# Kernel optimization log

Measured on AMD Instinct MI355X. Metric: run time of the kernel, lower is better.

Reference implementation:

```python
import jax, jax.numpy as jnp
import numpy as np

B, T, C, H = 4, 2048, 1024, 16


def setup_inputs() -> dict:
    key = jax.random.key(0)
    k0, k1, k2 = jax.random.split(key, 3)
    s = C ** -0.5
    return {
        "x": jax.random.normal(k0, (B, T, C), jnp.float32),
        "Wqkv": jax.random.normal(k1, (C, 3 * C), jnp.float32) * s,
        "bqkv": jnp.zeros((3 * C,), jnp.float32),
        "Wo": jax.random.normal(k2, (C, C), jnp.float32) * s,
        "bo": jnp.zeros((C,), jnp.float32),
        "decoder": 1,
    }


def reference(x, Wqkv, bqkv, Wo, bo, decoder):
    Bx, Tx, Cx = x.shape
    d = Cx // H  # head dim
    qkv = x @ Wqkv + bqkv  # [B,T,3C]
    q, k, v = jnp.split(qkv, 3, axis=-1)
    q = q.reshape(Bx, Tx, H, d).transpose(0, 2, 1, 3)  # [B,H,T,d]
    k = k.reshape(Bx, Tx, H, d).transpose(0, 2, 1, 3)
    v = v.reshape(Bx, Tx, H, d).transpose(0, 2, 1, 3)
    # Source: qk / embd_dim**(-0.5)  ==  qk * sqrt(embd_dim)  (faithful quirk)
    scale = jnp.asarray(Cx ** 0.5, x.dtype)
    qk = jnp.einsum("bhqd,bhkd->bhqk", q, k) * scale  # [B,H,T,T]
    if decoder:  # decoder is a Python int constant
        tril = jnp.tril(jnp.ones((Tx, Tx), bool))
        qk = jnp.where(tril, qk, -jnp.inf)
    attn = jax.nn.softmax(qk, axis=-1)
    out = jnp.einsum("bhqk,bhkd->bhqd", attn, v)  # [B,H,T,d]
    out = out.transpose(0, 2, 1, 3).reshape(Bx, Tx, Cx)
    return out @ Wo + bo
```

## Files before the change

kernel.cpp:

```cpp
#include <hip/hip_runtime.h>
#include <cstdint>
#include <cstddef>

#define T_SEQ 2048
#define CEMB  1024
#define NHEAD 16
#define DHEAD 64

#define QSCALE 46.1662413084468f

typedef __attribute__((ext_vector_type(8))) short bf16x8;
typedef __attribute__((ext_vector_type(4))) float f32x4;

static __device__ __forceinline__ unsigned short f2bf(float x) {
    unsigned u = __builtin_bit_cast(unsigned, x);
    unsigned r = (u + 0x7FFFu + ((u >> 16) & 1u)) >> 16;
    return (unsigned short)r;
}
static __device__ __forceinline__ float bf2f(unsigned short b) {
    unsigned u = ((unsigned)b) << 16;
    return __builtin_bit_cast(float, u);
}

static __device__ __forceinline__ void gload16(const short* gsrc, short* ldsbase) {
    __builtin_amdgcn_global_load_lds(
        (const __attribute__((address_space(1))) void*)gsrc,
        (__attribute__((address_space(3))) void*)ldsbase, 16, 0, 0);
}

__global__ __launch_bounds__(256) void split_x_kernel(
    const float* __restrict__ x, short* __restrict__ hi, short* __restrict__ lo)
{
    size_t base = ((size_t)blockIdx.x * 256 + threadIdx.x) * 8;
    float4 f0 = *(const float4*)(x + base);
    float4 f1 = *(const float4*)(x + base + 4);
    float xs[8] = {f0.x, f0.y, f0.z, f0.w, f1.x, f1.y, f1.z, f1.w};
    bf16x8 h8, l8;
    #pragma unroll
    for (int e = 0; e < 8; ++e) {
        unsigned u = __builtin_bit_cast(unsigned, xs[e]);
        h8[e] = (short)(unsigned short)(u >> 16);
        float hf = __builtin_bit_cast(float, u & 0xFFFF0000u);
        l8[e] = (short)f2bf(xs[e] - hf);
    }
    *(bf16x8*)(hi + base) = h8;
    *(bf16x8*)(lo + base) = l8;
}

__global__ __launch_bounds__(512) void gemm_qk_kernel(
    const short* __restrict__ Ah, const short* __restrict__ Al,
    const short* __restrict__ Bh, const short* __restrict__ Bl,
    const float* __restrict__ bias,
    short* __restrict__ Chi, short* __restrict__ Clo, int K)
{
    __shared__ __align__(16) short smem[24576];

    const int tid = threadIdx.x;
    const int wv = tid >> 6, l = tid & 63;
    const int lr = l & 15, lg = l >> 4;
    const int wr = wv >> 1, wc = wv & 1;
    const int row0 = blockIdx.y * 256;
    const int col0 = blockIdx.x * 128;

    f32x4 acc[4][4];
    #pragma unroll
    for (int mt = 0; mt < 4; ++mt)
        #pragma unroll
        for (int nt = 0; nt < 4; ++nt)
            acc[mt][nt] = (f32x4){0.f, 0.f, 0.f, 0.f};

    const int sA0 = wv * 128 + l, sA1 = sA0 + 64;
    const size_t aO0 = (size_t)(row0 + (sA0 & 255)) * K + (sA0 >> 8) * 8;
    const size_t aO1 = (size_t)(row0 + (sA1 & 255)) * K + (sA1 >> 8) * 8;
    const int sB = wv * 64 + l;
    const size_t bO = (size_t)(col0 + (sB & 127)) * K + (sB >> 7) * 8;

    const short* gAh0 = Ah + aO0;  const short* gAh1 = Ah + aO1;
    const short* gAl0 = Al + aO0;  const short* gAl1 = Al + aO1;
    const short* gBh  = Bh + bO;   const short* gBl  = Bl + bO;

    short* const dA0 = &smem[(wv * 128) * 8];
    short* const dA1 = &smem[(wv * 128 + 64) * 8];
    short* const dB  = &smem[16384 + (wv * 64) * 8];

    for (int kt = 0; kt < K; kt += 32) {
        __syncthreads();
        gload16(gAh0 + kt, dA0);
        gload16(gAh1 + kt, dA1);
        gload16(gAl0 + kt, dA0 + 8192);
        gload16(gAl1 + kt, dA1 + 8192);
        gload16(gBh + kt, dB);
        gload16(gBl + kt, dB + 4096);
        __syncthreads();

        const int ao = (lg * 256 + wr * 64 + lr) * 8;
        const int bo = 16384 + (lg * 128 + wc * 64 + lr) * 8;
        bf16x8 ahf[4], alf[4];
        #pragma unroll
        for (int mt = 0; mt < 4; ++mt) {
            ahf[mt] = *(const bf16x8*)&smem[ao + mt * 128];
            alf[mt] = *(const bf16x8*)&smem[8192 + ao + mt * 128];
        }
        #pragma unroll
        for (int nt = 0; nt < 4; ++nt) {
            bf16x8 bhf = *(const bf16x8*)&smem[bo + nt * 128];
            bf16x8 blf = *(const bf16x8*)&smem[4096 + bo + nt * 128];
            #pragma unroll
            for (int mt = 0; mt < 4; ++mt) {
                acc[mt][nt] = __builtin_amdgcn_mfma_f32_16x16x32_bf16(ahf[mt], bhf, acc[mt][nt], 0, 0, 0);
                acc[mt][nt] = __builtin_amdgcn_mfma_f32_16x16x32_bf16(alf[mt], bhf, acc[mt][nt], 0, 0, 0);
                acc[mt][nt] = __builtin_amdgcn_mfma_f32_16x16x32_bf16(ahf[mt], blf, acc[mt][nt], 0, 0, 0);
            }
        }
    }

    #pragma unroll
    for (int mt = 0; mt < 4; ++mt) {
        #pragma unroll
        for (int r = 0; r < 4; ++r) {
            int m = row0 + wr * 64 + mt * 16 + lg * 4 + r;
            #pragma unroll
            for (int nt = 0; nt < 4; ++nt) {
                int n = col0 + wc * 64 + nt * 16 + lr;
                float v = acc[mt][nt][r] + bias[n];
                if (n < 1024) v *= QSCALE;
                unsigned u = __builtin_bit_cast(unsigned, v);
                Chi[(size_t)m * 2048 + n] = (short)(unsigned short)(u >> 16);
                float hf = __builtin_bit_cast(float, u & 0xFFFF0000u);
                Clo[(size_t)m * 2048 + n] = (short)f2bf(v - hf);
            }
        }
    }
}

__global__ __launch_bounds__(256) void gemm_v_kernel(
    const short* __restrict__ Ah, const short* __restrict__ Bh,
    const float* __restrict__ bias, short* __restrict__ vt, int K)
{
    __shared__ __align__(16) short smem[17408];

    const int tid = threadIdx.x;
    const int w = tid >> 6, l = tid & 63;
    const int lr = l & 15, lg = l >> 4;
    const int wr = w >> 1, wc = w & 1;
    const int row0 = blockIdx.y * 128;
    const int col0 = blockIdx.x * 128;

    f32x4 acc[4][4];
    #pragma unroll
    for (int mt = 0; mt < 4; ++mt)
        #pragma unroll
        for (int nt = 0; nt < 4; ++nt)
            acc[mt][nt] = (f32x4){0.f, 0.f, 0.f, 0.f};

    const int s0 = w * 128 + l, s1 = s0 + 64;
    const size_t aoff0 = (size_t)(row0 + (s0 & 127)) * K + (s0 >> 7) * 8;
    const size_t aoff1 = (size_t)(row0 + (s1 & 127)) * K + (s1 >> 7) * 8;
    const size_t boff0 = (size_t)(col0 + (s0 & 127)) * K + (s0 >> 7) * 8;
    const size_t boff1 = (size_t)(col0 + (s1 & 127)) * K + (s1 >> 7) * 8;
    const short* gA0 = Ah + aoff0;  const short* gA1 = Ah + aoff1;
    const short* gB0 = Bh + boff0;  const short* gB1 = Bh + boff1;
    short* const dA0 = &smem[(w * 128) * 8];
    short* const dA1 = &smem[(w * 128 + 64) * 8];
    short* const dB0 = &smem[4096 + (w * 128) * 8];
    short* const dB1 = &smem[4096 + (w * 128 + 64) * 8];

    for (int kt = 0; kt < K; kt += 32) {
        __syncthreads();
        gload16(gA0 + kt, dA0);
        gload16(gA1 + kt, dA1);
        gload16(gB0 + kt, dB0);
        gload16(gB1 + kt, dB1);
        __syncthreads();

        const int ao = (lg * 128 + wr * 64 + lr) * 8;
        const int bo = 4096 + (lg * 128 + wc * 64 + lr) * 8;
        bf16x8 ahf[4];
        #pragma unroll
        for (int mt = 0; mt < 4; ++mt)
            ahf[mt] = *(const bf16x8*)&smem[ao + mt * 128];
        #pragma unroll
        for (int nt = 0; nt < 4; ++nt) {
            bf16x8 bhf = *(const bf16x8*)&smem[bo + nt * 128];
            #pragma unroll
            for (int mt = 0; mt < 4; ++mt)
                acc[mt][nt] = __builtin_amdgcn_mfma_f32_16x16x32_bf16(ahf[mt], bhf, acc[mt][nt], 0, 0, 0);
        }
    }

    __syncthreads();
    #pragma unroll
    for (int mt = 0; mt < 4; ++mt) {
        const int tb = wr * 64 + mt * 16 + lg * 4;
        #pragma unroll
        for (int nt = 0; nt < 4; ++nt) {
            const int nl = wc * 64 + nt * 16 + lr;
            float v0 = acc[mt][nt][0] + bias[col0 + nl];
            float v1 = acc[mt][nt][1] + bias[col0 + nl];
            float v2 = acc[mt][nt][2] + bias[col0 + nl];
            float v3 = acc[mt][nt][3] + bias[col0 + nl];
            unsigned u0 = (unsigned)f2bf(v0) | ((unsigned)f2bf(v1) << 16);
            unsigned u1 = (unsigned)f2bf(v2) | ((unsigned)f2bf(v3) << 16);
            uint2 uu; uu.x = u0; uu.y = u1;
            *(uint2*)&smem[nl * 136 + tb] = uu;
        }
    }
    __syncthreads();

    const int b  = row0 >> 11;
    const int t0 = row0 & 2047;
    #pragma unroll
    for (int i = 0; i < 8; ++i) {
        int nl = (tid >> 4) + i * 16;
        int t8 = (tid & 15) * 8;
        bf16x8 vv = *(const bf16x8*)&smem[nl * 136 + t8];
        int n = col0 + nl;
        int hh = n >> 6, d = n & 63;
        short* dst = vt + ((size_t)((b * NHEAD + hh) * DHEAD + d)) * T_SEQ + t0 + t8;
        *(bf16x8*)dst = vv;
    }
}

__global__ __launch_bounds__(256) void gemm_proj_kernel(
    const short* __restrict__ Ah, const short* __restrict__ Bh,
    const float* __restrict__ bias, float* __restrict__ Cout, int K, int ldc)
{
    __shared__ __align__(16) short smem[8192];

    const int tid = threadIdx.x;
    const int w = tid >> 6, l = tid & 63;
    const int lr = l & 15, lg = l >> 4;
    const int wr = w >> 1, wc = w & 1;
    const int row0 = blockIdx.y * 128;
    const int col0 = blockIdx.x * 128;

    f32x4 acc[4][4];
    #pragma unroll
    for (int mt = 0; mt < 4; ++mt)
        #pragma unroll
        for (int nt = 0; nt < 4; ++nt)
            acc[mt][nt] = (f32x4){0.f, 0.f, 0.f, 0.f};

    const int s0 = w * 128 + l, s1 = s0 + 64;
    const size_t aoff0 = (size_t)(row0 + (s0 & 127)) * K + (s0 >> 7) * 8;
    const size_t aoff1 = (size_t)(row0 + (s1 & 127)) * K + (s1 >> 7) * 8;
    const size_t boff0 = (size_t)(col0 + (s0 & 127)) * K + (s0 >> 7) * 8;
    const size_t boff1 = (size_t)(col0 + (s1 & 127)) * K + (s1 >> 7) * 8;
    const short* gA0 = Ah + aoff0;  const short* gA1 = Ah + aoff1;
    const short* gB0 = Bh + boff0;  const short* gB1 = Bh + boff1;
    short* const dA0 = &smem[(w * 128) * 8];
    short* const dA1 = &smem[(w * 128 + 64) * 8];
    short* const dB0 = &smem[4096 + (w * 128) * 8];
    short* const dB1 = &smem[4096 + (w * 128 + 64) * 8];

    for (int kt = 0; kt < K; kt += 32) {
        __syncthreads();
        gload16(gA0 + kt, dA0);
        gload16(gA1 + kt, dA1);
        gload16(gB0 + kt, dB0);
        gload16(gB1 + kt, dB1);
        __syncthreads();

        const int ao = (lg * 128 + wr * 64 + lr) * 8;
        const int bo = 4096 + (lg * 128 + wc * 64 + lr) * 8;
        bf16x8 ahf[4];
        #pragma unroll
        for (int mt = 0; mt < 4; ++mt)
            ahf[mt] = *(const bf16x8*)&smem[ao + mt * 128];
        #pragma unroll
        for (int nt = 0; nt < 4; ++nt) {
            bf16x8 bhf = *(const bf16x8*)&smem[bo + nt * 128];
            #pragma unroll
            for (int mt = 0; mt < 4; ++mt)
                acc[mt][nt] = __builtin_amdgcn_mfma_f32_16x16x32_bf16(ahf[mt], bhf, acc[mt][nt], 0, 0, 0);
        }
    }

    #pragma unroll
    for (int mt = 0; mt < 4; ++mt) {
        #pragma unroll
        for (int r = 0; r < 4; ++r) {
            int m = row0 + wr * 64 + mt * 16 + lg * 4 + r;
            #pragma unroll
            for (int nt = 0; nt < 4; ++nt) {
                int n = col0 + wc * 64 + nt * 16 + lr;
                Cout[(size_t)m * ldc + n] = acc[mt][nt][r] + bias[n];
            }
        }
    }
}

__global__ __launch_bounds__(256) void transpose_split_kernel(
    const float* __restrict__ src, int nsrc,
    short* __restrict__ hi, short* __restrict__ lo)
{
    __shared__ float tile[64][68];
    const int tid = threadIdx.x;
    const int n0 = blockIdx.x * 64, k0 = blockIdx.y * 64;
    {
        int kr = tid >> 2, cg = tid & 3;
        const float* s = src + (size_t)(k0 + kr) * nsrc + n0 + cg * 16;
        #pragma unroll
        for (int q = 0; q < 4; ++q) {
            float4 f = *(const float4*)(s + q * 4);
            tile[kr][cg * 16 + q * 4 + 0] = f.x;
            tile[kr][cg * 16 + q * 4 + 1] = f.y;
            tile[kr][cg * 16 + q * 4 + 2] = f.z;
            tile[kr][cg * 16 + q * 4 + 3] = f.w;
        }
    }
    __syncthreads();
    {
        int nr = tid >> 2, kg = tid & 3;
        int n = n0 + nr;
        bf16x8 h0, h1, lo0, lo1;
        #pragma unroll
        for (int e = 0; e < 8; ++e) {
            float a = tile[kg * 16 + e][nr];
            float b = tile[kg * 16 + 8 + e][nr];
            unsigned short ha = f2bf(a), hb = f2bf(b);
            h0[e] = (short)ha; h1[e] = (short)hb;
            lo0[e] = (short)f2bf(a - bf2f(ha));
            lo1[e] = (short)f2bf(b - bf2f(hb));
        }
        short* dh = hi + (size_t)n * 1024 + k0 + kg * 16;
        *(bf16x8*)dh = h0;
        *(bf16x8*)(dh + 8) = h1;
        if (lo) {
            short* dl = lo + (size_t)n * 1024 + k0 + kg * 16;
            *(bf16x8*)dl = lo0;
            *(bf16x8*)(dl + 8) = lo1;
        }
    }
}

__global__ __launch_bounds__(256) void attn_mfma_kernel(
    const short* __restrict__ qkhi, const short* __restrict__ qklo,
    const short* __restrict__ vt, short* __restrict__ ctxb)
{
    __shared__ __align__(16) short smem[20480];

    const int tid = threadIdx.x;
    const int w = tid >> 6, l = tid & 63;
    const int lr = l & 15, lg = l >> 4;

    const int bid = blockIdx.x;
    const int p  = bid >> 6;
    const int bh = bid & 63;
    const int h = bh & 15, b = bh >> 4;
    const size_t bT = (size_t)b * T_SEQ;

    const int g0 = w * 128 + l, g1 = g0 + 64;
    const int rg0 = g0 >> 3, rg1 = g1 >> 3;
    const int sc0 = (g0 & 7) ^ (rg0 & 7), sc1 = (g1 & 7) ^ (rg1 & 7);
    short* const dK0 = &smem[(w * 128) * 8];
    short* const dK1 = &smem[(w * 128 + 64) * 8];

    const size_t koff0 = (bT + rg0) * 2048 + 1024 + h * DHEAD + sc0 * 8;
    const size_t koff1 = (bT + rg1) * 2048 + 1024 + h * DHEAD + sc1 * 8;
    const short* const pKh0 = qkhi + koff0;
    const short* const pKh1 = qkhi + koff1;
    const short* const pKl0 = qklo + koff0;
    const short* const pKl1 = qklo + koff1;
    const short* const pV0 = vt + ((size_t)((b * NHEAD + h) * DHEAD) + rg0) * T_SEQ + sc0 * 8;
    const short* const pV1 = vt + ((size_t)((b * NHEAD + h) * DHEAD) + rg1) * T_SEQ + sc1 * 8;

    const int psBase = 16384 + w * 1024;
    const int pwChunk = (lg >> 1);
    const int pwIntra = (lg & 1) * 4;

    for (int half = 0; half < 2; ++half) {
        const int xi = half ? (31 - p) : p;
        const int qw = xi * 64 + w * 16;
        const int nsteps = xi + 1;

        __syncthreads();

        bf16x8 qhi[2], qlo[2];
        #pragma unroll
        for (int kk = 0; kk < 2; ++kk) {
            size_t off = (bT + qw + lr) * 2048 + h * DHEAD + kk * 32 + lg * 8;
            qhi[kk] = *(const bf16x8*)(qkhi + off);
            qlo[kk] = *(const bf16x8*)(qklo + off);
        }
        __builtin_amdgcn_sched_barrier(0);

        gload16(pKh0, dK0);
        gload16(pKh1, dK1);
        gload16(pKl0, dK0 + 4096);
        gload16(pKl1, dK1 + 4096);
        gload16(pV0, dK0 + 8192);
        gload16(pV1, dK1 + 8192);
        {
            int j1 = (nsteps > 1) ? 64 : 0;
            gload16(pV0 + j1, dK0 + 12288);
            gload16(pV1 + j1, dK1 + 12288);
        }

        f32x4 O[4];
        #pragma unroll
        for (int dt = 0; dt < 4; ++dt)
            O[dt] = (f32x4){0.f, 0.f, 0.f, 0.f};
        float mrow = -3.0e38f;
        float lrow = 0.f;

        for (int t = 0; t < nsteps; ++t) {
            const int j0 = t * 64;
            asm volatile("s_waitcnt vmcnt(2)" ::: "memory");
            __builtin_amdgcn_s_barrier();
            __builtin_amdgcn_sched_barrier(0);
            const int vbase = 8192 + (t & 1) * 4096;

            f32x4 St[4];
            __builtin_amdgcn_s_setprio(1);
            #pragma unroll
            for (int ct = 0; ct < 4; ++ct) {
                f32x4 s = (f32x4){0.f, 0.f, 0.f, 0.f};
                #pragma unroll
                for (int kk = 0; kk < 2; ++kk) {
                    int j  = ct * 16 + lr;
                    int ck = kk * 4 + lg;
                    int idx = j * 64 + ((ck ^ (j & 7)) << 3);
                    bf16x8 kh8 = *(bf16x8*)&smem[idx];
                    bf16x8 kl8 = *(bf16x8*)&smem[4096 + idx];
                    s = __builtin_amdgcn_mfma_f32_16x16x32_bf16(kh8, qhi[kk], s, 0, 0, 0);
                    s = __builtin_amdgcn_mfma_f32_16x16x32_bf16(kh8, qlo[kk], s, 0, 0, 0);
                    s = __builtin_amdgcn_mfma_f32_16x16x32_bf16(kl8, qhi[kk], s, 0, 0, 0);
                }
                St[ct] = s;
            }
            __builtin_amdgcn_s_setprio(0);
            #pragma unroll
            for (int ct = 0; ct < 4; ++ct) {
                if (j0 + ct * 16 + 15 > qw) {
                    #pragma unroll
                    for (int r = 0; r < 4; ++r) {
                        int jabs = j0 + ct * 16 + lg * 4 + r;
                        St[ct][r] = (jabs <= qw + lr) ? St[ct][r] : -3.0e38f;
                    }
                }
            }

            float tm = fmaxf(fmaxf(fmaxf(St[0][0], St[0][1]), fmaxf(St[0][2], St[0][3])),
                             fmaxf(fmaxf(St[1][0], St[1][1]), fmaxf(St[1][2], St[1][3])));
            tm = fmaxf(tm, fmaxf(fmaxf(fmaxf(St[2][0], St[2][1]), fmaxf(St[2][2], St[2][3])),
                                 fmaxf(fmaxf(St[3][0], St[3][1]), fmaxf(St[3][2], St[3][3]))));
            tm = fmaxf(tm, __shfl_xor(tm, 16));
            tm = fmaxf(tm, __shfl_xor(tm, 32));

            if (__any(tm > mrow)) {
                float mnew  = fmaxf(mrow, tm);
                float alpha = __builtin_amdgcn_exp2f(mrow - mnew);
                mrow = mnew;
                lrow *= alpha;
                #pragma unroll
                for (int r = 0; r < 4; ++r) {
                    float aO = __shfl(alpha, lg * 4 + r);
                    #pragma unroll
                    for (int dt = 0; dt < 4; ++dt)
                        O[dt][r] *= aO;
                }
            }

            #pragma unroll
            for (int ct = 0; ct < 4; ++ct) {
                float p0 = __builtin_amdgcn_exp2f(St[ct][0] - mrow);
                float p1 = __builtin_amdgcn_exp2f(St[ct][1] - mrow);
                float p2 = __builtin_amdgcn_exp2f(St[ct][2] - mrow);
                float p3 = __builtin_amdgcn_exp2f(St[ct][3] - mrow);
                lrow += (p0 + p1) + (p2 + p3);
                unsigned u0 = (__builtin_bit_cast(unsigned, p0) >> 16) |
                              (__builtin_bit_cast(unsigned, p1) & 0xFFFF0000u);
                unsigned u1 = (__builtin_bit_cast(unsigned, p2) >> 16) |
                              (__builtin_bit_cast(unsigned, p3) & 0xFFFF0000u);
                int chunk = ct * 2 + pwChunk;
                int sidx = psBase + lr * 64 + ((chunk ^ (lr & 7)) << 3) + pwIntra;
                uint2 uu; uu.x = u0; uu.y = u1;
                *(uint2*)&smem[sidx] = uu;
            }

            __builtin_amdgcn_wave_barrier();

            bf16x8 pa[2];
            #pragma unroll
            for (int jk = 0; jk < 2; ++jk) {
                int ck = jk * 4 + lg;
                pa[jk] = *(bf16x8*)&smem[psBase + lr * 64 + ((ck ^ (lr & 7)) << 3)];
            }
            __builtin_amdgcn_s_setprio(1);
            #pragma unroll
            for (int dt = 0; dt < 4; ++dt) {
                #pragma unroll
                for (int jk = 0; jk < 2; ++jk) {
                    int d  = dt * 16 + lr;
                    int ck = jk * 4 + lg;
                    bf16x8 vb = *(bf16x8*)&smem[vbase + d * 64 + ((ck ^ (d & 7)) << 3)];
                    O[dt] = __builtin_amdgcn_mfma_f32_16x16x32_bf16(pa[jk], vb, O[dt], 0, 0, 0);
                }
            }
            __builtin_amdgcn_s_setprio(0);

            __builtin_amdgcn_sched_barrier(0);
            __builtin_amdgcn_s_barrier();
            __builtin_amdgcn_sched_barrier(0);

            if (t + 1 < nsteps) {
                size_t ko = (size_t)(t + 1) * 131072;
                gload16(pKh0 + ko, dK0);
                gload16(pKh1 + ko, dK1);
                gload16(pKl0 + ko, dK0 + 4096);
                gload16(pKl1 + ko, dK1 + 4096);
                int jv = (t + 2 < nsteps) ? (t + 2) : (nsteps - 1);
                short* const dV = &smem[8192 + (t & 1) * 4096];
                gload16(pV0 + jv * 64, dV + (w * 128) * 8);
                gload16(pV1 + jv * 64, dV + (w * 128 + 64) * 8);
            }
        }

        float lsum = lrow + __shfl_xor(lrow, 16);
        lsum += __shfl_xor(lsum, 32);
        #pragma unroll
        for (int r = 0; r < 4; ++r) {
            float lO = __shfl(lsum, lg * 4 + r);
            float inv = 1.0f / lO;
            int row = qw + lg * 4 + r;
            #pragma unroll
            for (int dt = 0; dt < 4; ++dt) {
                int col = h * DHEAD + dt * 16 + lr;
                ctxb[(size_t)(b * T_SEQ + row) * CEMB + col] = (short)f2bf(O[dt][r] * inv);
            }
        }
    }
}

extern "C" void kernel_launch(void* const* d_in, const int* in_sizes, int n_in,
                              void* d_out, int out_size, void* d_ws, size_t ws_size,
                              hipStream_t stream)
{
    const float* x    = (const float*)d_in[0];
    const float* Wqkv = (const float*)d_in[1];
    const float* bqkv = (const float*)d_in[2];
    const float* Wo   = (const float*)d_in[3];
    const float* bo   = (const float*)d_in[4];
    float* out = (float*)d_out;

    char* ws = (char*)d_ws;
    short* qkhi = (short*)ws;
    short* qklo = (short*)(ws + (size_t)(32u << 20));
    short* xlo  = (short*)(ws + (size_t)(64u << 20));
    short* Vt   = xlo;
    short* xhi  = (short*)(ws + (size_t)(80u << 20));
    short* ctxb = xhi;
    short* WhiT = (short*)(ws + (size_t)(96u << 20));
    short* WloT = (short*)(ws + (size_t)(102u << 20));
    short* WoT  = (short*)(ws + (size_t)(108u << 20));

    transpose_split_kernel<<<dim3(48, 16), 256, 0, stream>>>(Wqkv, 3 * CEMB, WhiT, WloT);
    transpose_split_kernel<<<dim3(16, 16), 256, 0, stream>>>(Wo, CEMB, WoT, nullptr);

    split_x_kernel<<<dim3(4096), 256, 0, stream>>>(x, xhi, xlo);

    gemm_qk_kernel<<<dim3(16, 32), 512, 0, stream>>>(
        xhi, xlo, WhiT, WloT, bqkv, qkhi, qklo, CEMB);

    gemm_v_kernel<<<dim3(8, 64), 256, 0, stream>>>(
        xhi, WhiT + (size_t)2048 * 1024, bqkv + 2048, Vt, CEMB);

    attn_mfma_kernel<<<dim3(1024), 256, 0, stream>>>(qkhi, qklo, Vt, ctxb);

    gemm_proj_kernel<<<dim3(8, 64), 256, 0, stream>>>(
        ctxb, WoT, bo, out, CEMB, CEMB);
}
```

Baseline: 395.3 us.

## Fuse fp32-to-bf16 x split into QK and V GEMM loads; double-buffer projection GEMM

Removes the separate split_x kernel. The QK and V GEMMs now read fp32 x directly and convert it to bf16 hi/lo (or rounded bf16 for V) in registers before writing to LDS. This saves a full write and re-read of the split x buffers. The QK GEMM tile shrinks from 256x128 with 512 threads to 128x128 with 256 threads. The projection GEMM gains a two-stage LDS double buffer with explicit waitcnt and barriers so loads overlap MFMA work. The A-side loads are now synchronous register loads with conversion work in the k-loop, which may add latency because they are no longer async global-to-LDS.

```diff
diff --git a/kernel.cpp b/kernel.cpp
--- a/kernel.cpp
+++ b/kernel.cpp
@@ -28,38 +28,19 @@
         (__attribute__((address_space(3))) void*)ldsbase, 16, 0, 0);
 }
 
-__global__ __launch_bounds__(256) void split_x_kernel(
-    const float* __restrict__ x, short* __restrict__ hi, short* __restrict__ lo)
-{
-    size_t base = ((size_t)blockIdx.x * 256 + threadIdx.x) * 8;
-    float4 f0 = *(const float4*)(x + base);
-    float4 f1 = *(const float4*)(x + base + 4);
-    float xs[8] = {f0.x, f0.y, f0.z, f0.w, f1.x, f1.y, f1.z, f1.w};
-    bf16x8 h8, l8;
-    #pragma unroll
-    for (int e = 0; e < 8; ++e) {
-        unsigned u = __builtin_bit_cast(unsigned, xs[e]);
-        h8[e] = (short)(unsigned short)(u >> 16);
-        float hf = __builtin_bit_cast(float, u & 0xFFFF0000u);
-        l8[e] = (short)f2bf(xs[e] - hf);
-    }
-    *(bf16x8*)(hi + base) = h8;
-    *(bf16x8*)(lo + base) = l8;
-}
-
-__global__ __launch_bounds__(512) void gemm_qk_kernel(
-    const short* __restrict__ Ah, const short* __restrict__ Al,
+__global__ __launch_bounds__(256) void gemm_qk_kernel(
+    const float* __restrict__ Af,
     const short* __restrict__ Bh, const short* __restrict__ Bl,
     const float* __restrict__ bias,
     short* __restrict__ Chi, short* __restrict__ Clo, int K)
 {
-    __shared__ __align__(16) short smem[24576];
+    __shared__ __align__(16) short smem[16384];
 
     const int tid = threadIdx.x;
-    const int wv = tid >> 6, l = tid & 63;
+    const int w = tid >> 6, l = tid & 63;
     const int lr = l & 15, lg = l >> 4;
-    const int wr = wv >> 1, wc = wv & 1;
-    const int row0 = blockIdx.y * 256;
+    const int wr = w >> 1, wc = w & 1;
+    const int row0 = blockIdx.y * 128;
     const int col0 = blockIdx.x * 128;
 
     f32x4 acc[4][4];
@@ -69,32 +50,51 @@
         for (int nt = 0; nt < 4; ++nt)
             acc[mt][nt] = (f32x4){0.f, 0.f, 0.f, 0.f};
 
-    const int sA0 = wv * 128 + l, sA1 = sA0 + 64;
-    const size_t aO0 = (size_t)(row0 + (sA0 & 255)) * K + (sA0 >> 8) * 8;
-    const size_t aO1 = (size_t)(row0 + (sA1 & 255)) * K + (sA1 >> 8) * 8;
-    const int sB = wv * 64 + l;
-    const size_t bO = (size_t)(col0 + (sB & 127)) * K + (sB >> 7) * 8;
-
-    const short* gAh0 = Ah + aO0;  const short* gAh1 = Ah + aO1;
-    const short* gAl0 = Al + aO0;  const short* gAl1 = Al + aO1;
-    const short* gBh  = Bh + bO;   const short* gBl  = Bl + bO;
-
-    short* const dA0 = &smem[(wv * 128) * 8];
-    short* const dA1 = &smem[(wv * 128 + 64) * 8];
-    short* const dB  = &smem[16384 + (wv * 64) * 8];
+    const int sB0 = w * 128 + l, sB1 = sB0 + 64;
+    const size_t bO0 = (size_t)(col0 + (sB0 & 127)) * K + (sB0 >> 7) * 8;
+    const size_t bO1 = (size_t)(col0 + (sB1 & 127)) * K + (sB1 >> 7) * 8;
+    const short* gB0  = Bh + bO0;  const short* gB1  = Bh + bO1;
+    const short* gBl0 = Bl + bO0;  const short* gBl1 = Bl + bO1;
+    short* const dB0 = &smem[4096 + (w * 128) * 8];
+    short* const dB1 = &smem[4096 + (w * 128 + 64) * 8];
+
+    const int arow = tid >> 1, ahalf = tid & 1;
+    const float* gAf = Af + (size_t)(row0 + arow) * K + ahalf * 16;
 
     for (int kt = 0; kt < K; kt += 32) {
         __syncthreads();
-        gload16(gAh0 + kt, dA0);
-        gload16(gAh1 + kt, dA1);
-        gload16(gAl0 + kt, dA0 + 8192);
-        gload16(gAl1 + kt, dA1 + 8192);
-        gload16(gBh + kt, dB);
-        gload16(gBl + kt, dB + 4096);
+        gload16(gB0 + kt, dB0);
+        gload16(gB1 + kt, dB1);
+        gload16(gBl0 + kt, dB0 + 8192);
+        gload16(gBl1 + kt, dB1 + 8192);
+        {
+            const float* src = gAf + kt;
+            float4 f0 = *(const float4*)(src);
+            float4 f1 = *(const float4*)(src + 4);
+            float4 f2 = *(const float4*)(src + 8);
+            float4 f3 = *(const float4*)(src + 12);
+            float xs[16] = {f0.x, f0.y, f0.z, f0.w, f1.x, f1.y, f1.z, f1.w,
+                            f2.x, f2.y, f2.z, f2.w, f3.x, f3.y, f3.z, f3.w};
+            #pragma unroll
+            for (int q = 0; q < 2; ++q) {
+                bf16x8 h8, l8;
+                #pragma unroll
+                for (int e = 0; e < 8; ++e) {
+                    float x = xs[q * 8 + e];
+                    unsigned u = __builtin_bit_cast(unsigned, x);
+                    h8[e] = (short)(unsigned short)(u >> 16);
+                    float hf = __builtin_bit_cast(float, u & 0xFFFF0000u);
+                    l8[e] = (short)f2bf(x - hf);
+                }
+                int slot = (ahalf * 2 + q) * 128 + arow;
+                *(bf16x8*)&smem[slot * 8] = h8;
+                *(bf16x8*)&smem[8192 + slot * 8] = l8;
+            }
+        }
         __syncthreads();
 
-        const int ao = (lg * 256 + wr * 64 + lr) * 8;
-        const int bo = 16384 + (lg * 128 + wc * 64 + lr) * 8;
+        const int ao = (lg * 128 + wr * 64 + lr) * 8;
+        const int bo = 4096 + (lg * 128 + wc * 64 + lr) * 8;
         bf16x8 ahf[4], alf[4];
         #pragma unroll
         for (int mt = 0; mt < 4; ++mt) {
@@ -104,7 +104,7 @@
         #pragma unroll
         for (int nt = 0; nt < 4; ++nt) {
             bf16x8 bhf = *(const bf16x8*)&smem[bo + nt * 128];
-            bf16x8 blf = *(const bf16x8*)&smem[4096 + bo + nt * 128];
+            bf16x8 blf = *(const bf16x8*)&smem[8192 + bo + nt * 128];
             #pragma unroll
             for (int mt = 0; mt < 4; ++mt) {
                 acc[mt][nt] = __builtin_amdgcn_mfma_f32_16x16x32_bf16(ahf[mt], bhf, acc[mt][nt], 0, 0, 0);
@@ -134,10 +134,110 @@
 }
 
 __global__ __launch_bounds__(256) void gemm_v_kernel(
-    const short* __restrict__ Ah, const short* __restrict__ Bh,
+    const float* __restrict__ Af, const short* __restrict__ Bh,
     const float* __restrict__ bias, short* __restrict__ vt, int K)
 {
     __shared__ __align__(16) short smem[17408];
+
+    const int tid = threadIdx.x;
+    const int w = tid >> 6, l = tid & 63;
+    const int lr = l & 15, lg = l >> 4;
+    const int wr = w >> 1, wc = w & 1;
+    const int row0 = blockIdx.y * 128;
+    const int col0 = blockIdx.x * 128;
+
+    f32x4 acc[4][4];
+    #pragma unroll
+    for (int mt = 0; mt < 4; ++mt)
+        #pragma unroll
+        for (int nt = 0; nt < 4; ++nt)
+            acc[mt][nt] = (f32x4){0.f, 0.f, 0.f, 0.f};
+
+    const int sB0 = w * 128 + l, sB1 = sB0 + 64;
+    const size_t bO0 = (size_t)(col0 + (sB0 & 127)) * K + (sB0 >> 7) * 8;
+    const size_t bO1 = (size_t)(col0 + (sB1 & 127)) * K + (sB1 >> 7) * 8;
+    const short* gB0 = Bh + bO0;  const short* gB1 = Bh + bO1;
+    short* const dB0 = &smem[4096 + (w * 128) * 8];
+    short* const dB1 = &smem[4096 + (w * 128 + 64) * 8];
+
+    const int arow = tid >> 1, ahalf = tid & 1;
+    const float* gAf = Af + (size_t)(row0 + arow) * K + ahalf * 16;
+
+    for (int kt = 0; kt < K; kt += 32) {
+        __syncthreads();
+        gload16(gB0 + kt, dB0);
+        gload16(gB1 + kt, dB1);
+        {
+            const float* src = gAf + kt;
+            float4 f0 = *(const float4*)(src);
+            float4 f1 = *(const float4*)(src + 4);
+            float4 f2 = *(const float4*)(src + 8);
+            float4 f3 = *(const float4*)(src + 12);
+            float xs[16] = {f0.x, f0.y, f0.z, f0.w, f1.x, f1.y, f1.z, f1.w,
+                            f2.x, f2.y, f2.z, f2.w, f3.x, f3.y, f3.z, f3.w};
+            #pragma unroll
+            for (int q = 0; q < 2; ++q) {
+                bf16x8 h8;
+                #pragma unroll
+                for (int e = 0; e < 8; ++e) h8[e] = (short)f2bf(xs[q * 8 + e]);
+                int slot = (ahalf * 2 + q) * 128 + arow;
+                *(bf16x8*)&smem[slot * 8] = h8;
+            }
+        }
+        __syncthreads();
+
+        const int ao = (lg * 128 + wr * 64 + lr) * 8;
+        const int bo = 4096 + (lg * 128 + wc * 64 + lr) * 8;
+        bf16x8 ahf[4];
+        #pragma unroll
+        for (int mt = 0; mt < 4; ++mt)
+            ahf[mt] = *(const bf16x8*)&smem[ao + mt * 128];
+        #pragma unroll
+        for (int nt = 0; nt < 4; ++nt) {
+            bf16x8 bhf = *(const bf16x8*)&smem[bo + nt * 128];
+            #pragma unroll
+            for (int mt = 0; mt < 4; ++mt)
+                acc[mt][nt] = __builtin_amdgcn_mfma_f32_16x16x32_bf16(ahf[mt], bhf, acc[mt][nt], 0, 0, 0);
+        }
+    }
+
+    __syncthreads();
+    #pragma unroll
+    for (int mt = 0; mt < 4; ++mt) {
+        const int tb = wr * 64 + mt * 16 + lg * 4;
+        #pragma unroll
+        for (int nt = 0; nt < 4; ++nt) {
+            const int nl = wc * 64 + nt * 16 + lr;
+            float bv = bias[col0 + nl];
+            unsigned u0 = (unsigned)f2bf(acc[mt][nt][0] + bv) |
+                          ((unsigned)f2bf(acc[mt][nt][1] + bv) << 16);
+            unsigned u1 = (unsigned)f2bf(acc[mt][nt][2] + bv) |
+                          ((unsigned)f2bf(acc[mt][nt][3] + bv) << 16);
+            uint2 uu; uu.x = u0; uu.y = u1;
+            *(uint2*)&smem[nl * 136 + tb] = uu;
+        }
+    }
+    __syncthreads();
+
+    const int b  = row0 >> 11;
+    const int t0 = row0 & 2047;
+    #pragma unroll
+    for (int i = 0; i < 8; ++i) {
+        int nl = (tid >> 4) + i * 16;
+        int t8 = (tid & 15) * 8;
+        bf16x8 vv = *(const bf16x8*)&smem[nl * 136 + t8];
+        int n = col0 + nl;
+        int hh = n >> 6, d = n & 63;
+        short* dst = vt + ((size_t)((b * NHEAD + hh) * DHEAD + d)) * T_SEQ + t0 + t8;
+        *(bf16x8*)dst = vv;
+    }
+}
+
+__global__ __launch_bounds__(256) void gemm_proj_kernel(
+    const short* __restrict__ Ah, const short* __restrict__ Bh,
+    const float* __restrict__ bias, float* __restrict__ Cout, int K, int ldc)
+{
+    __shared__ __align__(16) short smem[16384];
 
     const int tid = threadIdx.x;
     const int w = tid >> 6, l = tid & 63;
@@ -165,16 +265,28 @@
     short* const dB0 = &smem[4096 + (w * 128) * 8];
     short* const dB1 = &smem[4096 + (w * 128 + 64) * 8];
 
-    for (int kt = 0; kt < K; kt += 32) {
-        __syncthreads();
-        gload16(gA0 + kt, dA0);
-        gload16(gA1 + kt, dA1);
-        gload16(gB0 + kt, dB0);
-        gload16(gB1 + kt, dB1);
-        __syncthreads();
-
-        const int ao = (lg * 128 + wr * 64 + lr) * 8;
-        const int bo = 4096 + (lg * 128 + wc * 64 + lr) * 8;
+    #define PSTAGE(buf, kt) do {                      \
+        gload16(gA0 + (kt), dA0 + (buf) * 8192);      \
+        gload16(gA1 + (kt), dA1 + (buf) * 8192);      \
+        gload16(gB0 + (kt), dB0 + (buf) * 8192);      \
+        gload16(gB1 + (kt), dB1 + (buf) * 8192);      \
+    } while (0)
+
+    const int nkt = K / 32;
+    PSTAGE(0, 0);
+    for (int ti = 0; ti < nkt; ++ti) {
+        if (ti + 1 < nkt) {
+            PSTAGE((ti + 1) & 1, (ti + 1) * 32);
+            asm volatile("s_waitcnt vmcnt(4)" ::: "memory");
+        } else {
+            asm volatile("s_waitcnt vmcnt(0)" ::: "memory");
+        }
+        __builtin_amdgcn_s_barrier();
+        __builtin_amdgcn_sched_barrier(0);
+
+        const int sb = (ti & 1) * 8192;
+        const int ao = sb + (lg * 128 + wr * 64 + lr) * 8;
+        const int bo = sb + 4096 + (lg * 128 + wc * 64 + lr) * 8;
         bf16x8 ahf[4];
         #pragma unroll
         for (int mt = 0; mt < 4; ++mt)
@@ -186,95 +298,11 @@
             for (int mt = 0; mt < 4; ++mt)
                 acc[mt][nt] = __builtin_amdgcn_mfma_f32_16x16x32_bf16(ahf[mt], bhf, acc[mt][nt], 0, 0, 0);
         }
-    }
-
-    __syncthreads();
-    #pragma unroll
-    for (int mt = 0; mt < 4; ++mt) {
-        const int tb = wr * 64 + mt * 16 + lg * 4;
-        #pragma unroll
-        for (int nt = 0; nt < 4; ++nt) {
-            const int nl = wc * 64 + nt * 16 + lr;
-            float v0 = acc[mt][nt][0] + bias[col0 + nl];
-            float v1 = acc[mt][nt][1] + bias[col0 + nl];
-            float v2 = acc[mt][nt][2] + bias[col0 + nl];
-            float v3 = acc[mt][nt][3] + bias[col0 + nl];
-            unsigned u0 = (unsigned)f2bf(v0) | ((unsigned)f2bf(v1) << 16);
-            unsigned u1 = (unsigned)f2bf(v2) | ((unsigned)f2bf(v3) << 16);
-            uint2 uu; uu.x = u0; uu.y = u1;
-            *(uint2*)&smem[nl * 136 + tb] = uu;
-        }
-    }
-    __syncthreads();
-
-    const int b  = row0 >> 11;
-    const int t0 = row0 & 2047;
-    #pragma unroll
-    for (int i = 0; i < 8; ++i) {
-        int nl = (tid >> 4) + i * 16;
-        int t8 = (tid & 15) * 8;
-        bf16x8 vv = *(const bf16x8*)&smem[nl * 136 + t8];
-        int n = col0 + nl;
-        int hh = n >> 6, d = n & 63;
-        short* dst = vt + ((size_t)((b * NHEAD + hh) * DHEAD + d)) * T_SEQ + t0 + t8;
-        *(bf16x8*)dst = vv;
-    }
-}
-
-__global__ __launch_bounds__(256) void gemm_proj_kernel(
-    const short* __restrict__ Ah, const short* __restrict__ Bh,
-    const float* __restrict__ bias, float* __restrict__ Cout, int K, int ldc)
-{
-    __shared__ __align__(16) short smem[8192];
-
-    const int tid = threadIdx.x;
-    const int w = tid >> 6, l = tid & 63;
-    const int lr = l & 15, lg = l >> 4;
-    const int wr = w >> 1, wc = w & 1;
-    const int row0 = blockIdx.y * 128;
-    const int col0 = blockIdx.x * 128;
-
-    f32x4 acc[4][4];
-    #pragma unroll
-    for (int mt = 0; mt < 4; ++mt)
-        #pragma unroll
-        for (int nt = 0; nt < 4; ++nt)
-            acc[mt][nt] = (f32x4){0.f, 0.f, 0.f, 0.f};
-
-    const int s0 = w * 128 + l, s1 = s0 + 64;
-    const size_t aoff0 = (size_t)(row0 + (s0 & 127)) * K + (s0 >> 7) * 8;
-    const size_t aoff1 = (size_t)(row0 + (s1 & 127)) * K + (s1 >> 7) * 8;
-    const size_t boff0 = (size_t)(col0 + (s0 & 127)) * K + (s0 >> 7) * 8;
-    const size_t boff1 = (size_t)(col0 + (s1 & 127)) * K + (s1 >> 7) * 8;
-    const short* gA0 = Ah + aoff0;  const short* gA1 = Ah + aoff1;
-    const short* gB0 = Bh + boff0;  const short* gB1 = Bh + boff1;
-    short* const dA0 = &smem[(w * 128) * 8];
-    short* const dA1 = &smem[(w * 128 + 64) * 8];
-    short* const dB0 = &smem[4096 + (w * 128) * 8];
-    short* const dB1 = &smem[4096 + (w * 128 + 64) * 8];
-
-    for (int kt = 0; kt < K; kt += 32) {
-        __syncthreads();
-        gload16(gA0 + kt, dA0);
-        gload16(gA1 + kt, dA1);
-        gload16(gB0 + kt, dB0);
-        gload16(gB1 + kt, dB1);
-        __syncthreads();
-
-        const int ao = (lg * 128 + wr * 64 + lr) * 8;
-        const int bo = 4096 + (lg * 128 + wc * 64 + lr) * 8;
-        bf16x8 ahf[4];
-        #pragma unroll
-        for (int mt = 0; mt < 4; ++mt)
-            ahf[mt] = *(const bf16x8*)&smem[ao + mt * 128];
-        #pragma unroll
-        for (int nt = 0; nt < 4; ++nt) {
-            bf16x8 bhf = *(const bf16x8*)&smem[bo + nt * 128];
-            #pragma unroll
-            for (int mt = 0; mt < 4; ++mt)
-                acc[mt][nt] = __builtin_amdgcn_mfma_f32_16x16x32_bf16(ahf[mt], bhf, acc[mt][nt], 0, 0, 0);
-        }
-    }
+        __builtin_amdgcn_sched_barrier(0);
+        __builtin_amdgcn_s_barrier();
+        __builtin_amdgcn_sched_barrier(0);
+    }
+    #undef PSTAGE
 
     #pragma unroll
     for (int mt = 0; mt < 4; ++mt) {
@@ -547,10 +575,8 @@
     char* ws = (char*)d_ws;
     short* qkhi = (short*)ws;
     short* qklo = (short*)(ws + (size_t)(32u << 20));
-    short* xlo  = (short*)(ws + (size_t)(64u << 20));
-    short* Vt   = xlo;
-    short* xhi  = (short*)(ws + (size_t)(80u << 20));
-    short* ctxb = xhi;
+    short* Vt   = (short*)(ws + (size_t)(64u << 20));
+    short* ctxb = (short*)(ws + (size_t)(80u << 20));
     short* WhiT = (short*)(ws + (size_t)(96u << 20));
     short* WloT = (short*)(ws + (size_t)(102u << 20));
     short* WoT  = (short*)(ws + (size_t)(108u << 20));
@@ -558,13 +584,11 @@
     transpose_split_kernel<<<dim3(48, 16), 256, 0, stream>>>(Wqkv, 3 * CEMB, WhiT, WloT);
     transpose_split_kernel<<<dim3(16, 16), 256, 0, stream>>>(Wo, CEMB, WoT, nullptr);
 
-    split_x_kernel<<<dim3(4096), 256, 0, stream>>>(x, xhi, xlo);
-
-    gemm_qk_kernel<<<dim3(16, 32), 512, 0, stream>>>(
-        xhi, xlo, WhiT, WloT, bqkv, qkhi, qklo, CEMB);
+    gemm_qk_kernel<<<dim3(16, 64), 256, 0, stream>>>(
+        x, WhiT, WloT, bqkv, qkhi, qklo, CEMB);
 
     gemm_v_kernel<<<dim3(8, 64), 256, 0, stream>>>(
-        xhi, WhiT + (size_t)2048 * 1024, bqkv + 2048, Vt, CEMB);
+        x, WhiT + (size_t)2048 * 1024, bqkv + 2048, Vt, CEMB);
 
     attn_mfma_kernel<<<dim3(1024), 256, 0, stream>>>(qkhi, qklo, Vt, ctxb);
 
```

Measured after the change: 329.6 us. 16.6% less time.
